# Kernel tuning notes

Measured on AMD Instinct MI355X. Metric: run time of the kernel, lower is better.

Reference implementation:

```python
import jax, jax.numpy as jnp
import numpy as np

N_NODES = 10000
N_EDGES = 320000
D_IN = 256
D_HID = 256
N_TASKS = 128
N_GRAPHS = 128


def gcn_conv(x, W, b, src, dst, inv_sqrt_deg, n_nodes):
    # PyG GCNConv: x' = W x, then symmetric-normalized scatter-add over
    # edges (self-loops already included in src/dst), plus bias.
    h = x @ W  # [N, D_out]
    norm = inv_sqrt_deg[src] * inv_sqrt_deg[dst]  # [E+N]
    msg = h[src] * norm[:, None]  # [E+N, D_out] gathered messages
    out = jax.ops.segment_sum(msg, dst, num_segments=n_nodes)
    return out + b


def setup_inputs() -> dict:
    key = jax.random.key(0)
    ks = jax.random.split(key, 10)
    x = jax.random.normal(ks[0], (N_NODES, D_IN), dtype=jnp.float32)
    edge_index = jax.random.randint(ks[1], (2, N_EDGES), 0, N_NODES, dtype=jnp.int64)
    batch = jnp.sort(jax.random.randint(ks[2], (N_NODES,), 0, N_GRAPHS, dtype=jnp.int64))
    s = 1.0 / np.sqrt(D_HID)
    W1 = jax.random.uniform(ks[3], (D_IN, D_HID), jnp.float32, -s, s)
    b1 = jnp.zeros((D_HID,), jnp.float32)
    W2 = jax.random.uniform(ks[4], (D_HID, D_HID), jnp.float32, -s, s)
    b2 = jnp.zeros((D_HID,), jnp.float32)
    W3 = jax.random.uniform(ks[5], (D_HID, D_HID), jnp.float32, -s, s)
    b3 = jnp.zeros((D_HID,), jnp.float32)
    lin_w = jax.random.uniform(ks[6], (D_HID, N_TASKS), jnp.float32, -s, s)
    lin_b = jax.random.uniform(ks[7], (N_TASKS,), jnp.float32, -s, s)
    return {"x": x, "edge_index": edge_index, "batch": batch,
            "W1": W1, "b1": b1, "W2": W2, "b2": b2, "W3": W3, "b3": b3,
            "lin_w": lin_w, "lin_b": lin_b}


def reference(x, edge_index, batch, W1, b1, W2, b2, W3, b3, lin_w, lin_b):
    n = x.shape[0]
    loops = jnp.arange(n, dtype=edge_index.dtype)
    src = jnp.concatenate([edge_index[0], loops])  # add self-loops
    dst = jnp.concatenate([edge_index[1], loops])
    deg = jax.ops.segment_sum(jnp.ones_like(dst, dtype=x.dtype), dst, num_segments=n)
    inv_sqrt_deg = jnp.where(deg > 0, jax.lax.rsqrt(jnp.maximum(deg, 1.0)), 0.0)

    h = jax.nn.relu(gcn_conv(x, W1, b1, src, dst, inv_sqrt_deg, n))
    h = jax.nn.relu(gcn_conv(h, W2, b2, src, dst, inv_sqrt_deg, n))
    h = jax.nn.relu(gcn_conv(h, W3, b3, src, dst, inv_sqrt_deg, n))

    # global_mean_pool over graph ids
    sums = jax.ops.segment_sum(h, batch, num_segments=N_GRAPHS)  # [G, D]
    counts = jax.ops.segment_sum(jnp.ones((n,), h.dtype), batch, num_segments=N_GRAPHS)
    pooled = sums / jnp.maximum(counts, 1.0)[:, None]
    return pooled @ lin_w + lin_b  # [G, num_tasks]
```

## Files before the change

### kernel.cpp

```cpp
#include <hip/hip_runtime.h>

#define N_NODES  10000
#define N_EDGES  320000
#define D        256
#define N_TASKS  128
#define N_GRAPHS 128

#define CSR_BLOCKS 256
#define EPB (N_EDGES / CSR_BLOCKS)
#define MM_BX 157
#define MM_BLOCKS (MM_BX * 4)
#define SCAT_BLOCKS ((N_EDGES + 255) / 256)

typedef __attribute__((ext_vector_type(8))) _Float16 half8;
typedef __attribute__((ext_vector_type(4))) float floatx4;

__device__ __forceinline__ unsigned short f2h(float f) {
    _Float16 h = (_Float16)f;
    return *(unsigned short*)&h;
}
__device__ __forceinline__ float h2f(unsigned short u) {
    _Float16 h = *(_Float16*)&u;
    return (float)h;
}


__global__ __launch_bounds__(256) void prep_kernel(const int* __restrict__ dst,
                                                   unsigned short* __restrict__ histbuf,
                                                   unsigned short* __restrict__ rank,
                                                   const float* __restrict__ W1,
                                                   const float* __restrict__ W2,
                                                   const float* __restrict__ W3,
                                                   unsigned short* __restrict__ wt) {
    __shared__ int h[N_NODES];
    __shared__ float t[32][33];
    int t0 = threadIdx.x;
    if (blockIdx.x < CSR_BLOCKS) {
        int b = blockIdx.x;
        for (int i = t0; i < N_NODES; i += 256) h[i] = 0;
        __syncthreads();
        int e0 = b * EPB;
        for (int i = t0; i < EPB; i += 256) {
            int e = e0 + i;
            int r = atomicAdd(&h[dst[e]], 1);
            rank[e] = (unsigned short)r;
        }
        __syncthreads();
        int* outp = (int*)(histbuf + (size_t)b * N_NODES);
        for (int i = t0; i < N_NODES / 2; i += 256)
            outp[i] = (h[2 * i] & 0xffff) | (h[2 * i + 1] << 16);
    } else {
        int b = blockIdx.x - CSR_BLOCKS;
        int w = b >> 6, tile = b & 63;
        int kt = (tile >> 3) << 5, nt = (tile & 7) << 5;
        const float* W = (w == 0) ? W1 : (w == 1) ? W2 : W3;
        int r = t0 >> 5, c = t0 & 31;
#pragma unroll
        for (int i = 0; i < 4; ++i)
            t[r + 8 * i][c] = W[(size_t)(kt + r + 8 * i) * D + nt + c];
        __syncthreads();
        unsigned short* oh = wt + w * D * D;
#pragma unroll
        for (int i = 0; i < 4; ++i)
            oh[(size_t)(nt + r + 8 * i) * D + kt + c] = f2h(t[c][r + 8 * i]);
    }
}


__global__ __launch_bounds__(256) void merge_kernel(unsigned short* __restrict__ histbuf,
                                                    int* __restrict__ cnt) {
    int n = blockIdx.x * 256 + threadIdx.x;
    if (n >= N_NODES) return;
    int run = 0;
#pragma unroll 1
    for (int b = 0; b < CSR_BLOCKS; b += 8) {
        int v0 = histbuf[(size_t)(b + 0) * N_NODES + n];
        int v1 = histbuf[(size_t)(b + 1) * N_NODES + n];
        int v2 = histbuf[(size_t)(b + 2) * N_NODES + n];
        int v3 = histbuf[(size_t)(b + 3) * N_NODES + n];
        int v4 = histbuf[(size_t)(b + 4) * N_NODES + n];
        int v5 = histbuf[(size_t)(b + 5) * N_NODES + n];
        int v6 = histbuf[(size_t)(b + 6) * N_NODES + n];
        int v7 = histbuf[(size_t)(b + 7) * N_NODES + n];
        histbuf[(size_t)(b + 0) * N_NODES + n] = (unsigned short)run; run += v0;
        histbuf[(size_t)(b + 1) * N_NODES + n] = (unsigned short)run; run += v1;
        histbuf[(size_t)(b + 2) * N_NODES + n] = (unsigned short)run; run += v2;
        histbuf[(size_t)(b + 3) * N_NODES + n] = (unsigned short)run; run += v3;
        histbuf[(size_t)(b + 4) * N_NODES + n] = (unsigned short)run; run += v4;
        histbuf[(size_t)(b + 5) * N_NODES + n] = (unsigned short)run; run += v5;
        histbuf[(size_t)(b + 6) * N_NODES + n] = (unsigned short)run; run += v6;
        histbuf[(size_t)(b + 7) * N_NODES + n] = (unsigned short)run; run += v7;
    }
    cnt[n] = run + 1;
}


__global__ __launch_bounds__(256) void scan_kernel(const int* __restrict__ cnt,
                                                   int* __restrict__ rowptr,
                                                   float* __restrict__ isd) {
    __shared__ int scnt[10240];
    __shared__ int part[256];
    const int CH = 40;
    int t = threadIdx.x;
    for (int i = t; i < 2500; i += 256) ((int4*)scnt)[i] = ((const int4*)cnt)[i];
    for (int i = 10000 + t; i < 10240; i += 256) scnt[i] = 1;
    __syncthreads();
    int base = t * CH;
    int s = 0;
#pragma unroll 8
    for (int i = 0; i < CH; ++i) s += scnt[base + i] - 1;
    part[t] = s;
    __syncthreads();
    for (int off = 1; off < 256; off <<= 1) {
        int v = (t >= off) ? part[t - off] : 0;
        __syncthreads();
        part[t] += v;
        __syncthreads();
    }
    int run = (t == 0) ? 0 : part[t - 1];
    for (int i = 0; i < CH; ++i) {
        int idx = base + i;
        if (idx < N_NODES) {
            rowptr[idx] = run;
            int c = scnt[idx];
            run += c - 1;
            isd[idx] = rsqrtf((float)c);
        }
    }
    if (t == 255) rowptr[N_NODES] = run;
}


template <int F32IN>
__device__ __forceinline__ void mm_body(unsigned short (*sA)[40], unsigned short (*sW)[40],
                                        const void* __restrict__ Av,
                                        const unsigned short* __restrict__ Wt,
                                        unsigned short* __restrict__ C,
                                        int row0, int n0, int tid) {
    int lane = tid & 63, wid = tid >> 6;
    int wr = wid >> 1, wc = wid & 1;

    int sr = tid >> 2;
    int sk = (tid & 3) << 3;
    int arow = row0 + sr; if (arow >= N_NODES) arow = N_NODES - 1;
    const float*          pAf = (const float*)Av + (size_t)arow * D + sk;
    const unsigned short* pAh = (const unsigned short*)Av + (size_t)arow * D + sk;
    const unsigned short* pW  = Wt + (size_t)(n0 + sr) * D + sk;

    float4 rf0, rf1; uint4 rAh;
    if (F32IN) { rf0 = *(const float4*)pAf; rf1 = *(const float4*)(pAf + 4); }
    else       { rAh = *(const uint4*)pAh; }
    uint4 rW = *(const uint4*)pW;

    int fr = lane & 15;
    int fk = (lane >> 4) << 3;

    floatx4 acc00 = {0.f, 0.f, 0.f, 0.f};
    floatx4 acc01 = acc00, acc10 = acc00, acc11 = acc00;

#pragma unroll 1
    for (int step = 0; step < D / 32; ++step) {
        if (F32IN) {
            float vv[8] = {rf0.x, rf0.y, rf0.z, rf0.w, rf1.x, rf1.y, rf1.z, rf1.w};
            union { unsigned short u[8]; uint4 v; } ph;
#pragma unroll
            for (int j = 0; j < 8; ++j) ph.u[j] = f2h(vv[j]);
            *(uint4*)&sA[sr][sk] = ph.v;
        } else {
            *(uint4*)&sA[sr][sk] = rAh;
        }
        *(uint4*)&sW[sr][sk] = rW;
        __syncthreads();
        if (step < D / 32 - 1) {
            if (F32IN) {
                rf0 = *(const float4*)(pAf + (step + 1) * 32);
                rf1 = *(const float4*)(pAf + (step + 1) * 32 + 4);
            } else {
                rAh = *(const uint4*)(pAh + (step + 1) * 32);
            }
            rW = *(const uint4*)(pW + (step + 1) * 32);
        }
        half8 a0 = *(const half8*)&sA[(wr << 5) + fr][fk];
        half8 a1 = *(const half8*)&sA[(wr << 5) + 16 + fr][fk];
        half8 b0 = *(const half8*)&sW[(wc << 5) + fr][fk];
        half8 b1 = *(const half8*)&sW[(wc << 5) + 16 + fr][fk];
        acc00 = __builtin_amdgcn_mfma_f32_16x16x32_f16(a0, b0, acc00, 0, 0, 0);
        acc01 = __builtin_amdgcn_mfma_f32_16x16x32_f16(a0, b1, acc01, 0, 0, 0);
        acc10 = __builtin_amdgcn_mfma_f32_16x16x32_f16(a1, b0, acc10, 0, 0, 0);
        acc11 = __builtin_amdgcn_mfma_f32_16x16x32_f16(a1, b1, acc11, 0, 0, 0);
        __syncthreads();
    }

    int crow = (lane >> 4) << 2;
    int colbase = n0 + (wc << 5) + fr;
#pragma unroll
    for (int r = 0; r < 4; ++r) {
        int gr0 = row0 + (wr << 5) + crow + r;
        if (gr0 < N_NODES) {
            C[(size_t)gr0 * D + colbase]      = f2h(acc00[r]);
            C[(size_t)gr0 * D + colbase + 16] = f2h(acc01[r]);
        }
        int gr1 = gr0 + 16;
        if (gr1 < N_NODES) {
            C[(size_t)gr1 * D + colbase]      = f2h(acc10[r]);
            C[(size_t)gr1 * D + colbase + 16] = f2h(acc11[r]);
        }
    }
}

template <int F32IN>
__global__ __launch_bounds__(256) void mm_kernel(const void* __restrict__ Av,
                                                 const unsigned short* __restrict__ Wt,
                                                 unsigned short* __restrict__ C) {
    __shared__ unsigned short sA[64][40], sW[64][40];
    mm_body<F32IN>(sA, sW, Av, Wt, C, blockIdx.x << 6, blockIdx.y << 6, threadIdx.x);
}

__global__ __launch_bounds__(256) void scatmm_kernel(const float* __restrict__ x,
                                                     const unsigned short* __restrict__ Wt,
                                                     unsigned short* __restrict__ C,
                                                     const int* __restrict__ src,
                                                     const int* __restrict__ dst,
                                                     const unsigned short* __restrict__ rank,
                                                     const int* __restrict__ rowptr,
                                                     const unsigned short* __restrict__ histbuf,
                                                     const float* __restrict__ isd,
                                                     int2* __restrict__ edat) {
    __shared__ unsigned short sA[64][40], sW[64][40];
    if (blockIdx.x < MM_BLOCKS) {
        int row0 = (blockIdx.x % MM_BX) << 6;
        int n0   = (blockIdx.x / MM_BX) << 6;
        mm_body<1>(sA, sW, x, Wt, C, row0, n0, threadIdx.x);
    } else {
        int e = (blockIdx.x - MM_BLOCKS) * 256 + threadIdx.x;
        if (e < N_EDGES) {
            int b = e / EPB;
            int s = src[e], d = dst[e];
            int pos = rowptr[d] + (int)histbuf[(size_t)b * N_NODES + d] + (int)rank[e];
            edat[pos] = make_int2(s, __float_as_int(isd[s] * isd[d]));
        }
    }
}

__device__ __forceinline__ void fma8(uint4 q, float wt, float* acc) {
    acc[0] = fmaf(h2f((unsigned short)(q.x & 0xffff)), wt, acc[0]);
    acc[1] = fmaf(h2f((unsigned short)(q.x >> 16)),    wt, acc[1]);
    acc[2] = fmaf(h2f((unsigned short)(q.y & 0xffff)), wt, acc[2]);
    acc[3] = fmaf(h2f((unsigned short)(q.y >> 16)),    wt, acc[3]);
    acc[4] = fmaf(h2f((unsigned short)(q.z & 0xffff)), wt, acc[4]);
    acc[5] = fmaf(h2f((unsigned short)(q.z >> 16)),    wt, acc[5]);
    acc[6] = fmaf(h2f((unsigned short)(q.w & 0xffff)), wt, acc[6]);
    acc[7] = fmaf(h2f((unsigned short)(q.w >> 16)),    wt, acc[7]);
}

__global__ __launch_bounds__(256) void agg_kernel(const unsigned short* __restrict__ h,
                                                  const int* __restrict__ rowptr,
                                                  const int2* __restrict__ edat,
                                                  const float* __restrict__ isd,
                                                  const float* __restrict__ bias,
                                                  unsigned short* __restrict__ outh) {
    int node = (blockIdx.x * blockDim.x + threadIdx.x) >> 6;
    if (node >= N_NODES) return;
    int lane = threadIdx.x & 63;
    int half = lane >> 5;
    int sub  = lane & 31;

    float acc[8] = {0.f, 0.f, 0.f, 0.f, 0.f, 0.f, 0.f, 0.f};

    float isd_i = isd[node];
    float selfw = half ? 0.f : isd_i * isd_i;
    uint4 qs = *(const uint4*)(h + (size_t)node * D + (sub << 3));
    fma8(qs, selfw, acc);

    int e0 = rowptr[node];
    int deg = rowptr[node + 1] - e0;
    for (int base = 0; base < deg; base += 64) {
        int n = deg - base; if (n > 64) n = 64;
        int2 ed = edat[e0 + base + ((lane < n) ? lane : 0)];
        int pairs = (n + 1) >> 1;
        for (int p0 = 0; p0 < pairs; p0 += 8) {
            uint4 q[8]; float wt[8];
#pragma unroll
            for (int u = 0; u < 8; ++u) {
                int idx = ((p0 + u) << 1) + half;
                int idc = (idx < n) ? idx : 0;
                int s = __shfl(ed.x, idc);
                wt[u] = (idx < n && (p0 + u) < pairs)
                            ? __int_as_float(__shfl(ed.y, idc)) : 0.f;
                q[u] = *(const uint4*)(h + (size_t)s * D + (sub << 3));
            }
#pragma unroll
            for (int u = 0; u < 8; ++u) fma8(q[u], wt[u], acc);
        }
    }

#pragma unroll
    for (int i = 0; i < 8; ++i) acc[i] += __shfl_xor(acc[i], 32);

    if (half == 0) {
        const float* bp = bias + (sub << 3);
        float4 b0 = *(const float4*)bp;
        float4 b1 = *(const float4*)(bp + 4);
        float r0 = fmaxf(acc[0] + b0.x, 0.f), r1 = fmaxf(acc[1] + b0.y, 0.f);
        float r2 = fmaxf(acc[2] + b0.z, 0.f), r3 = fmaxf(acc[3] + b0.w, 0.f);
        float r4 = fmaxf(acc[4] + b1.x, 0.f), r5 = fmaxf(acc[5] + b1.y, 0.f);
        float r6 = fmaxf(acc[6] + b1.z, 0.f), r7 = fmaxf(acc[7] + b1.w, 0.f);
        uint4 o;
        o.x = (unsigned)f2h(r0) | ((unsigned)f2h(r1) << 16);
        o.y = (unsigned)f2h(r2) | ((unsigned)f2h(r3) << 16);
        o.z = (unsigned)f2h(r4) | ((unsigned)f2h(r5) << 16);
        o.w = (unsigned)f2h(r6) | ((unsigned)f2h(r7) << 16);
        *(uint4*)(outh + (size_t)node * D + (sub << 3)) = o;
    }
}

__global__ __launch_bounds__(256) void poolfinal_kernel(const unsigned short* __restrict__ h,
                                                        const int* __restrict__ batch,
                                                        const float* __restrict__ lw,
                                                        const float* __restrict__ lb,
                                                        float* __restrict__ out) {
    __shared__ float part[4][D];
    __shared__ float p[D];
    int g = blockIdx.x;
    int tid = threadIdx.x, w = tid >> 6, lane = tid & 63;
    int lo = 0, hi = N_NODES;
    while (lo < hi) { int m = (lo + hi) >> 1; if (batch[m] < g) lo = m + 1; else hi = m; }
    int start = lo;
    hi = N_NODES;
    while (lo < hi) { int m = (lo + hi) >> 1; if (batch[m] <= g) lo = m + 1; else hi = m; }
    int end = lo;
    float4 acc = make_float4(0.f, 0.f, 0.f, 0.f);
    for (int nd = start + w; nd < end; nd += 4) {
        ushort4 q = reinterpret_cast<const ushort4*>(h + (size_t)nd * D)[lane];
        acc.x += h2f(q.x); acc.y += h2f(q.y); acc.z += h2f(q.z); acc.w += h2f(q.w);
    }
    reinterpret_cast<float4*>(part[w])[lane] = acc;
    __syncthreads();
    float invc = 1.f / (float)((end > start) ? (end - start) : 1);
    p[tid] = (part[0][tid] + part[1][tid] + part[2][tid] + part[3][tid]) * invc;
    __syncthreads();
    if (tid < N_TASKS) {
        float a = lb[tid];
        for (int k = 0; k < D; ++k) a = fmaf(p[k], lw[k * N_TASKS + tid], a);
        out[g * N_TASKS + tid] = a;
    }
}

extern "C" void kernel_launch(void* const* d_in, const int* in_sizes, int n_in,
                              void* d_out, int out_size, void* d_ws, size_t ws_size,
                              hipStream_t stream) {
    const float* x   = (const float*)d_in[0];
    const int*   ei  = (const int*)d_in[1];
    const int*   bat = (const int*)d_in[2];
    const float* W1  = (const float*)d_in[3];
    const float* b1  = (const float*)d_in[4];
    const float* W2  = (const float*)d_in[5];
    const float* b2  = (const float*)d_in[6];
    const float* W3  = (const float*)d_in[7];
    const float* b3  = (const float*)d_in[8];
    const float* lw  = (const float*)d_in[9];
    const float* lb  = (const float*)d_in[10];
    float* out = (float*)d_out;

    const int* src = ei;
    const int* dst = ei + N_EDGES;

    char* ws = (char*)d_ws;
    unsigned short* gH      = (unsigned short*)(ws + 0);
    unsigned short* hH      = (unsigned short*)(ws + 5120000);
    unsigned short* Wt      = (unsigned short*)(ws + 10240000);
    float*          isd     = (float*)         (ws + 10633216);
    int*            cnt     = (int*)           (ws + 10673216);
    int*            rowptr  = (int*)           (ws + 10713216);
    int2*           edat    = (int2*)          (ws + 10753232);
    unsigned short* histbuf = (unsigned short*)(ws + 13313232);
    unsigned short* rank    = (unsigned short*)(ws + 18433232);

    prep_kernel<<<CSR_BLOCKS + 192, 256, 0, stream>>>(dst, histbuf, rank, W1, W2, W3, Wt);
    merge_kernel<<<(N_NODES + 255) / 256, 256, 0, stream>>>(histbuf, cnt);
    scan_kernel<<<1, 256, 0, stream>>>(cnt, rowptr, isd);
    scatmm_kernel<<<MM_BLOCKS + SCAT_BLOCKS, 256, 0, stream>>>(x, Wt, hH, src, dst, rank,
                                                               rowptr, histbuf, isd, edat);

    dim3 mmgrid(MM_BX, D / 64);
    const int AGG_BLOCKS = N_NODES / 4;

    agg_kernel<<<AGG_BLOCKS, 256, 0, stream>>>(hH, rowptr, edat, isd, b1, gH);
    mm_kernel<0><<<mmgrid, 256, 0, stream>>>(gH, Wt + D * D, hH);
    agg_kernel<<<AGG_BLOCKS, 256, 0, stream>>>(hH, rowptr, edat, isd, b2, gH);
    mm_kernel<0><<<mmgrid, 256, 0, stream>>>(gH, Wt + 2 * D * D, hH);
    agg_kernel<<<AGG_BLOCKS, 256, 0, stream>>>(hH, rowptr, edat, isd, b3, gH);
    poolfinal_kernel<<<N_GRAPHS, 256, 0, stream>>>(gH, bat, lw, lb, out);
}
```

Baseline: 139.6 us.

## Replace single-block scan with atomic segment allocation inside merge kernel

```diff
diff --git a/kernel.cpp b/kernel.cpp
--- a/kernel.cpp
+++ b/kernel.cpp
@@ -31,10 +31,12 @@
                                                    const float* __restrict__ W1,
                                                    const float* __restrict__ W2,
                                                    const float* __restrict__ W3,
-                                                   unsigned short* __restrict__ wt) {
+                                                   unsigned short* __restrict__ wt,
+                                                   int* __restrict__ gcount) {
     __shared__ int h[N_NODES];
     __shared__ float t[32][33];
     int t0 = threadIdx.x;
+    if (blockIdx.x == 0 && t0 == 0) *gcount = 0;
     if (blockIdx.x < CSR_BLOCKS) {
         int b = blockIdx.x;
         for (int i = t0; i < N_NODES; i += 256) h[i] = 0;
@@ -66,68 +68,70 @@
     }
 }
 
-
 __global__ __launch_bounds__(256) void merge_kernel(unsigned short* __restrict__ histbuf,
-                                                    int* __restrict__ cnt) {
-    int n = blockIdx.x * 256 + threadIdx.x;
-    if (n >= N_NODES) return;
-    int run = 0;
+                                                    int* __restrict__ rowptr,
+                                                    int* __restrict__ deg,
+                                                    float* __restrict__ isd,
+                                                    int* __restrict__ gcount) {
+    __shared__ int lds_p[64][4];
+    __shared__ int lds_b[64][4];
+    int t = threadIdx.x;
+    int ng = t >> 2, part = t & 3;
+    int node = blockIdx.x * 64 + ng;
+    bool valid = node < N_NODES;
+    int psum = 0;
+    if (valid) {
+        const unsigned short* col = histbuf + node;
 #pragma unroll 1
-    for (int b = 0; b < CSR_BLOCKS; b += 8) {
-        int v0 = histbuf[(size_t)(b + 0) * N_NODES + n];
-        int v1 = histbuf[(size_t)(b + 1) * N_NODES + n];
-        int v2 = histbuf[(size_t)(b + 2) * N_NODES + n];
-        int v3 = histbuf[(size_t)(b + 3) * N_NODES + n];
-        int v4 = histbuf[(size_t)(b + 4) * N_NODES + n];
-        int v5 = histbuf[(size_t)(b + 5) * N_NODES + n];
-        int v6 = histbuf[(size_t)(b + 6) * N_NODES + n];
-        int v7 = histbuf[(size_t)(b + 7) * N_NODES + n];
-        histbuf[(size_t)(b + 0) * N_NODES + n] = (unsigned short)run; run += v0;
-        histbuf[(size_t)(b + 1) * N_NODES + n] = (unsigned short)run; run += v1;
-        histbuf[(size_t)(b + 2) * N_NODES + n] = (unsigned short)run; run += v2;
-        histbuf[(size_t)(b + 3) * N_NODES + n] = (unsigned short)run; run += v3;
-        histbuf[(size_t)(b + 4) * N_NODES + n] = (unsigned short)run; run += v4;
-        histbuf[(size_t)(b + 5) * N_NODES + n] = (unsigned short)run; run += v5;
-        histbuf[(size_t)(b + 6) * N_NODES + n] = (unsigned short)run; run += v6;
-        histbuf[(size_t)(b + 7) * N_NODES + n] = (unsigned short)run; run += v7;
-    }
-    cnt[n] = run + 1;
-}
-
-
-__global__ __launch_bounds__(256) void scan_kernel(const int* __restrict__ cnt,
-                                                   int* __restrict__ rowptr,
-                                                   float* __restrict__ isd) {
-    __shared__ int scnt[10240];
-    __shared__ int part[256];
-    const int CH = 40;
-    int t = threadIdx.x;
-    for (int i = t; i < 2500; i += 256) ((int4*)scnt)[i] = ((const int4*)cnt)[i];
-    for (int i = 10000 + t; i < 10240; i += 256) scnt[i] = 1;
+        for (int r = 0; r < 64; r += 8) {
+            int b = (part << 6) + r;
+            int v0 = col[(size_t)(b + 0) * N_NODES];
+            int v1 = col[(size_t)(b + 1) * N_NODES];
+            int v2 = col[(size_t)(b + 2) * N_NODES];
+            int v3 = col[(size_t)(b + 3) * N_NODES];
+            int v4 = col[(size_t)(b + 4) * N_NODES];
+            int v5 = col[(size_t)(b + 5) * N_NODES];
+            int v6 = col[(size_t)(b + 6) * N_NODES];
+            int v7 = col[(size_t)(b + 7) * N_NODES];
+            psum += v0 + v1 + v2 + v3 + v4 + v5 + v6 + v7;
+        }
+    }
+    lds_p[ng][part] = psum;
     __syncthreads();
-    int base = t * CH;
-    int s = 0;
-#pragma unroll 8
-    for (int i = 0; i < CH; ++i) s += scnt[base + i] - 1;
-    part[t] = s;
+    if (valid && part == 0) {
+        int p0 = lds_p[ng][0], p1 = lds_p[ng][1], p2 = lds_p[ng][2], p3 = lds_p[ng][3];
+        int d = p0 + p1 + p2 + p3;
+        rowptr[node] = atomicAdd(gcount, d);
+        deg[node] = d;
+        isd[node] = rsqrtf((float)(d + 1));
+        lds_b[ng][0] = 0; lds_b[ng][1] = p0;
+        lds_b[ng][2] = p0 + p1; lds_b[ng][3] = p0 + p1 + p2;
+    }
     __syncthreads();
-    for (int off = 1; off < 256; off <<= 1) {
-        int v = (t >= off) ? part[t - off] : 0;
-        __syncthreads();
-        part[t] += v;
-        __syncthreads();
-    }
-    int run = (t == 0) ? 0 : part[t - 1];
-    for (int i = 0; i < CH; ++i) {
-        int idx = base + i;
-        if (idx < N_NODES) {
-            rowptr[idx] = run;
-            int c = scnt[idx];
-            run += c - 1;
-            isd[idx] = rsqrtf((float)c);
-        }
-    }
-    if (t == 255) rowptr[N_NODES] = run;
+    if (valid) {
+        int run = lds_b[ng][part];
+        unsigned short* col = histbuf + node;
+#pragma unroll 1
+        for (int r = 0; r < 64; r += 8) {
+            int b = (part << 6) + r;
+            int v0 = col[(size_t)(b + 0) * N_NODES];
+            int v1 = col[(size_t)(b + 1) * N_NODES];
+            int v2 = col[(size_t)(b + 2) * N_NODES];
+            int v3 = col[(size_t)(b + 3) * N_NODES];
+            int v4 = col[(size_t)(b + 4) * N_NODES];
+            int v5 = col[(size_t)(b + 5) * N_NODES];
+            int v6 = col[(size_t)(b + 6) * N_NODES];
+            int v7 = col[(size_t)(b + 7) * N_NODES];
+            col[(size_t)(b + 0) * N_NODES] = (unsigned short)run; run += v0;
+            col[(size_t)(b + 1) * N_NODES] = (unsigned short)run; run += v1;
+            col[(size_t)(b + 2) * N_NODES] = (unsigned short)run; run += v2;
+            col[(size_t)(b + 3) * N_NODES] = (unsigned short)run; run += v3;
+            col[(size_t)(b + 4) * N_NODES] = (unsigned short)run; run += v4;
+            col[(size_t)(b + 5) * N_NODES] = (unsigned short)run; run += v5;
+            col[(size_t)(b + 6) * N_NODES] = (unsigned short)run; run += v6;
+            col[(size_t)(b + 7) * N_NODES] = (unsigned short)run; run += v7;
+        }
+    }
 }
 
 
@@ -253,12 +257,13 @@
     acc[7] = fmaf(h2f((unsigned short)(q.w >> 16)),    wt, acc[7]);
 }
 
-__global__ __launch_bounds__(256) void agg_kernel(const unsigned short* __restrict__ h,
-                                                  const int* __restrict__ rowptr,
-                                                  const int2* __restrict__ edat,
-                                                  const float* __restrict__ isd,
-                                                  const float* __restrict__ bias,
-                                                  unsigned short* __restrict__ outh) {
+__global__ __launch_bounds__(256, 6) void agg_kernel(const unsigned short* __restrict__ h,
+                                                     const int* __restrict__ rowptr,
+                                                     const int* __restrict__ degv,
+                                                     const int2* __restrict__ edat,
+                                                     const float* __restrict__ isd,
+                                                     const float* __restrict__ bias,
+                                                     unsigned short* __restrict__ outh) {
     int node = (blockIdx.x * blockDim.x + threadIdx.x) >> 6;
     if (node >= N_NODES) return;
     int lane = threadIdx.x & 63;
@@ -273,7 +278,7 @@
     fma8(qs, selfw, acc);
 
     int e0 = rowptr[node];
-    int deg = rowptr[node + 1] - e0;
+    int deg = degv[node];
     for (int base = 0; base < deg; base += 64) {
         int n = deg - base; if (n > 64) n = 64;
         int2 ed = edat[e0 + base + ((lane < n) ? lane : 0)];
@@ -370,25 +375,26 @@
     unsigned short* hH      = (unsigned short*)(ws + 5120000);
     unsigned short* Wt      = (unsigned short*)(ws + 10240000);
     float*          isd     = (float*)         (ws + 10633216);
-    int*            cnt     = (int*)           (ws + 10673216);
+    int*            deg     = (int*)           (ws + 10673216);
     int*            rowptr  = (int*)           (ws + 10713216);
     int2*           edat    = (int2*)          (ws + 10753232);
     unsigned short* histbuf = (unsigned short*)(ws + 13313232);
     unsigned short* rank    = (unsigned short*)(ws + 18433232);
-
-    prep_kernel<<<CSR_BLOCKS + 192, 256, 0, stream>>>(dst, histbuf, rank, W1, W2, W3, Wt);
-    merge_kernel<<<(N_NODES + 255) / 256, 256, 0, stream>>>(histbuf, cnt);
-    scan_kernel<<<1, 256, 0, stream>>>(cnt, rowptr, isd);
+    int*            gcount  = (int*)           (ws + 19073232);
+
+    prep_kernel<<<CSR_BLOCKS + 192, 256, 0, stream>>>(dst, histbuf, rank, W1, W2, W3, Wt,
+                                                      gcount);
+    merge_kernel<<<(N_NODES + 63) / 64, 256, 0, stream>>>(histbuf, rowptr, deg, isd, gcount);
     scatmm_kernel<<<MM_BLOCKS + SCAT_BLOCKS, 256, 0, stream>>>(x, Wt, hH, src, dst, rank,
                                                                rowptr, histbuf, isd, edat);
 
     dim3 mmgrid(MM_BX, D / 64);
     const int AGG_BLOCKS = N_NODES / 4;
 
-    agg_kernel<<<AGG_BLOCKS, 256, 0, stream>>>(hH, rowptr, edat, isd, b1, gH);
+    agg_kernel<<<AGG_BLOCKS, 256, 0, stream>>>(hH, rowptr, deg, edat, isd, b1, gH);
     mm_kernel<0><<<mmgrid, 256, 0, stream>>>(gH, Wt + D * D, hH);
-    agg_kernel<<<AGG_BLOCKS, 256, 0, stream>>>(hH, rowptr, edat, isd, b2, gH);
+    agg_kernel<<<AGG_BLOCKS, 256, 0, stream>>>(hH, rowptr, deg, edat, isd, b2, gH);
     mm_kernel<0><<<mmgrid, 256, 0, stream>>>(gH, Wt + 2 * D * D, hH);
-    agg_kernel<<<AGG_BLOCKS, 256, 0, stream>>>(hH, rowptr, edat, isd, b3, gH);
+    agg_kernel<<<AGG_BLOCKS, 256, 0, stream>>>(hH, rowptr, deg, edat, isd, b3, gH);
     poolfinal_kernel<<<N_GRAPHS, 256, 0, stream>>>(gH, bat, lw, lb, out);
 }
```

After: 219.6 us. +57.3%, slower.
